# Kernel tuning notes

Hardware: AMD Instinct MI355X
Metric: run time of the kernel (lower is better)

The kernel has to match this reference:

```python
import jax, jax.numpy as jnp
import numpy as np

DIM = 1024
N_HEAD = 16
HEAD_DIM = DIM // N_HEAD
B, T = 2, 2048


def setup_inputs() -> dict:
    key = jax.random.key(0)
    ks = jax.random.split(key, 9)
    s = 1.0 / np.sqrt(DIM)
    return {
        "x": jax.random.normal(ks[0], (B, T, DIM), dtype=jnp.float32),
        "Wq": jax.random.normal(ks[1], (DIM, DIM), dtype=jnp.float32) * s,
        "bq": jax.random.normal(ks[2], (DIM,), dtype=jnp.float32) * s,
        "Wk": jax.random.normal(ks[3], (DIM, DIM), dtype=jnp.float32) * s,
        "bk": jax.random.normal(ks[4], (DIM,), dtype=jnp.float32) * s,
        "Wv": jax.random.normal(ks[5], (DIM, DIM), dtype=jnp.float32) * s,
        "bv": jax.random.normal(ks[6], (DIM,), dtype=jnp.float32) * s,
        "Wo": jax.random.normal(ks[7], (DIM, DIM), dtype=jnp.float32) * s,
        "bo": jax.random.normal(ks[8], (DIM,), dtype=jnp.float32) * s,
    }


def reference(x, Wq, bq, Wk, bk, Wv, bv, Wo, bo):
    b, t, d = x.shape
    # torch nn.Linear: y = x @ W.T + b
    Q = x @ Wq.T + bq  # [b, t, d]
    K = x @ Wk.T + bk
    V = x @ Wv.T + bv
    # split heads -> [b, h, t, hd]
    Q = Q.reshape(b, t, N_HEAD, HEAD_DIM).transpose(0, 2, 1, 3)
    K = K.reshape(b, t, N_HEAD, HEAD_DIM).transpose(0, 2, 1, 3)
    V = V.reshape(b, t, N_HEAD, HEAD_DIM).transpose(0, 2, 1, 3)
    scale = 1.0 / jnp.sqrt(jnp.float32(HEAD_DIM))
    score = jnp.einsum('bhqd,bhkd->bhqk', Q, K) * scale  # [b, h, t, t]
    attn = jax.nn.softmax(score, axis=-1)
    # dropout is identity in eval mode
    out = jnp.einsum('bhqk,bhkd->bhqd', attn, V)  # [b, h, t, hd]
    out = out.transpose(0, 2, 1, 3).reshape(b, t, d)
    return out @ Wo.T + bo
```

## Files before the change

### kernel.cpp

```cpp
#include <hip/hip_runtime.h>


#define DIM 1024
#define NH 16
#define HD 64
#define SEQ 2048
#define NROWS 4096
#define NT 32

typedef unsigned short u16;
typedef unsigned int u32;
typedef __bf16 bf16_t;
typedef bf16_t bf16x8 __attribute__((ext_vector_type(8)));
typedef float f32x4 __attribute__((ext_vector_type(4)));
typedef u16 u16x4 __attribute__((ext_vector_type(4)));
typedef u32 u32x2 __attribute__((ext_vector_type(2)));

typedef const __attribute__((address_space(1))) void* gas_ptr;
typedef __attribute__((address_space(3))) void* las_ptr;

#define S_BARRIER() asm volatile("s_barrier" ::: "memory")
#define S_WAITCNT_VM(N) asm volatile("s_waitcnt vmcnt(" #N ")" ::: "memory")

__device__ __forceinline__ void gl_lds16(const void* g, void* lds_wave_base) {
  __builtin_amdgcn_global_load_lds((gas_ptr)g, (las_ptr)lds_wave_base, 16, 0, 0);
}

__device__ __forceinline__ f32x4 mfma_bf16(bf16x8 a, bf16x8 b, f32x4 c) {
  return __builtin_amdgcn_mfma_f32_16x16x32_bf16(a, b, c, 0, 0, 0);
}

__device__ __forceinline__ u32 cvtpk(float lo, float hi) {
  u32 r;
  asm("v_cvt_pk_bf16_f32 %0, %1, %2" : "=v"(r) : "v"(lo), "v"(hi));
  return r;
}

__device__ __forceinline__ u16 bfu(float f) {
  bf16_t b = (bf16_t)f;
  union { bf16_t b; u16 u; } cv; cv.b = b; return cv.u;
}

__device__ __forceinline__ float fexp2(float x) {
#if __has_builtin(__builtin_amdgcn_exp2f)
  return __builtin_amdgcn_exp2f(x);
#else
  return exp2f(x);
#endif
}

#define QSCALE 0.18033688f

__global__ void cvt_all(const float* __restrict__ x,
                        const float* __restrict__ wq, const float* __restrict__ wk,
                        const float* __restrict__ wv, const float* __restrict__ wo,
                        u16* __restrict__ xb,
                        u16* __restrict__ oq, u16* __restrict__ ok,
                        u16* __restrict__ ov, u16* __restrict__ oo) {
  const int bid = blockIdx.x;
  const float* in;
  u16* out;
  float s = 1.0f;
  int off;
  if (bid < 4096) {
    in = x; out = xb; off = bid;
  } else {
    const int wi = (bid - 4096) >> 10;
    off = (bid - 4096) & 1023;
    in = wi == 0 ? wq : wi == 1 ? wk : wi == 2 ? wv : wo;
    out = wi == 0 ? oq : wi == 1 ? ok : wi == 2 ? ov : oo;
    if (wi == 0) s = QSCALE;
  }
  const int i = off * 256 + threadIdx.x;
  float4 v = ((const float4*)in)[i];
  u16x4 o;
  o.x = bfu(v.x * s); o.y = bfu(v.y * s); o.z = bfu(v.z * s); o.w = bfu(v.w * s);
  ((u16x4*)out)[i] = o;
}

__device__ __forceinline__ int xcd_swz(int L, int nwg) {
  return (L & 7) * (nwg >> 3) + (L >> 3);
}

__global__ __launch_bounds__(256, 3) void gemm_qkv(const u16* __restrict__ A,
                                                   const u16* __restrict__ wq,
                                                   const u16* __restrict__ wk,
                                                   const u16* __restrict__ wv,
                                                   const float* __restrict__ bq,
                                                   const float* __restrict__ bk,
                                                   const float* __restrict__ bv,
                                                   u16* __restrict__ Qb,
                                                   u16* __restrict__ Kb,
                                                   u16* __restrict__ Vtb) {
  __shared__ u16 As[3][128 * 32];
  __shared__ u16 Bs[3][128 * 32];
  const int L = blockIdx.y * gridDim.x + blockIdx.x;
  const int swz = xcd_swz(L, gridDim.x * gridDim.y);
  const int bx = swz % gridDim.x, by = swz / gridDim.x;
  const int which = bx >> 3;
  const int col0 = (bx & 7) * 128;
  const u16* W = which == 0 ? wq : which == 1 ? wk : wv;
  const float* bias = which == 0 ? bq : which == 1 ? bk : bv;
  const float bscale = which == 0 ? QSCALE : 1.0f;

  const int t = threadIdx.x, lane = t & 63, w = t >> 6;
  const int row0 = by * 128;
  const int wr = w >> 1, wc = w & 1;
  const int lr = lane & 15, lk = lane >> 4;

  f32x4 acc[4][4] = {};

  auto stage = [&](int k0, int bu) {
#pragma unroll
    for (int i = 0; i < 2; ++i) {
      const int bc = i * 256 + w * 64;
      const int f = bc + lane;
      gl_lds16(A + (size_t)(row0 + (f >> 2)) * DIM + k0 + (f & 3) * 8, &As[bu][bc * 8]);
      gl_lds16(W + (size_t)(col0 + (f >> 2)) * DIM + k0 + (f & 3) * 8, &Bs[bu][bc * 8]);
    }
  };

  stage(0, 0);
  stage(32, 1);
  int bcur = 0, bst = 2;
  for (int k = 0; k < 32; ++k) {
    S_BARRIER();
    if (k + 2 < 32) { stage((k + 2) * 32, bst); S_WAITCNT_VM(8); }
    else if (k + 1 < 32) { S_WAITCNT_VM(4); }
    else { S_WAITCNT_VM(0); }
    S_BARRIER();

    bf16x8 a[4], b[4];
#pragma unroll
    for (int m = 0; m < 4; ++m)
      a[m] = *(const bf16x8*)&As[bcur][(wr * 64 + m * 16 + lr) * 32 + lk * 8];
#pragma unroll
    for (int n = 0; n < 4; ++n)
      b[n] = *(const bf16x8*)&Bs[bcur][(wc * 64 + n * 16 + lr) * 32 + lk * 8];
    __builtin_amdgcn_s_setprio(1);
#pragma unroll
    for (int m = 0; m < 4; ++m)
#pragma unroll
      for (int n = 0; n < 4; ++n)
        acc[m][n] = mfma_bf16(a[m], b[n], acc[m][n]);
    __builtin_amdgcn_s_setprio(0);

    bcur = bcur == 2 ? 0 : bcur + 1;
    bst = bst == 2 ? 0 : bst + 1;
  }

#pragma unroll
  for (int m = 0; m < 4; ++m) {
    const int rowb = row0 + wr * 64 + m * 16 + lk * 4;
#pragma unroll
    for (int n = 0; n < 4; ++n) {
      const int ocol = col0 + wc * 64 + n * 16 + lr;
      const float bc = bias[ocol] * bscale;
      if (which != 2) {
        u16* dst = which == 0 ? Qb : Kb;
#pragma unroll
        for (int r = 0; r < 4; ++r)
          dst[(size_t)(rowb + r) * DIM + ocol] = bfu(acc[m][n][r] + bc);
      } else {
        u16x4 pk;
#pragma unroll
        for (int r = 0; r < 4; ++r) pk[r] = bfu(acc[m][n][r] + bc);
        const size_t idx = ((((size_t)(rowb >> 11) * NH + (ocol >> 6)) * HD + (ocol & 63)) << 11) + (rowb & 2047);
        *(u16x4*)&Vtb[idx] = pk;
      }
    }
  }
}

__global__ __launch_bounds__(256, 2) void gemm_out(const u16* __restrict__ A,
                                                   const u16* __restrict__ W,
                                                   const float* __restrict__ bias,
                                                   float* __restrict__ C) {
  __shared__ u16 As[3][64 * 32];
  __shared__ u16 Bs[3][128 * 32];
  const int L = blockIdx.x;
  const int swz = xcd_swz(L, 512);
  const int row0 = (swz >> 3) * 64, col0 = (swz & 7) * 128;
  const int t = threadIdx.x, lane = t & 63, w = t >> 6;
  const int wr = w >> 1, wc = w & 1;
  const int lr = lane & 15, lk = lane >> 4;

  f32x4 acc[2][4] = {};

  auto stage = [&](int k0, int bu) {
    const int fa = w * 64 + lane;
    gl_lds16(A + (size_t)(row0 + (fa >> 2)) * DIM + k0 + (fa & 3) * 8, &As[bu][w * 512]);
#pragma unroll
    for (int i = 0; i < 2; ++i) {
      const int bc = i * 256 + w * 64;
      const int fb = bc + lane;
      gl_lds16(W + (size_t)(col0 + (fb >> 2)) * DIM + k0 + (fb & 3) * 8, &Bs[bu][bc * 8]);
    }
  };

  stage(0, 0);
  stage(32, 1);
  int bcur = 0, bst = 2;
  for (int k = 0; k < 32; ++k) {
    S_BARRIER();
    if (k + 2 < 32) { stage((k + 2) * 32, bst); S_WAITCNT_VM(6); }
    else if (k + 1 < 32) { S_WAITCNT_VM(3); }
    else { S_WAITCNT_VM(0); }
    S_BARRIER();

    bf16x8 a[2], b[4];
#pragma unroll
    for (int m = 0; m < 2; ++m)
      a[m] = *(const bf16x8*)&As[bcur][(wr * 32 + m * 16 + lr) * 32 + lk * 8];
#pragma unroll
    for (int n = 0; n < 4; ++n)
      b[n] = *(const bf16x8*)&Bs[bcur][(wc * 64 + n * 16 + lr) * 32 + lk * 8];
    __builtin_amdgcn_s_setprio(1);
#pragma unroll
    for (int m = 0; m < 2; ++m)
#pragma unroll
      for (int n = 0; n < 4; ++n)
        acc[m][n] = mfma_bf16(a[m], b[n], acc[m][n]);
    __builtin_amdgcn_s_setprio(0);

    bcur = bcur == 2 ? 0 : bcur + 1;
    bst = bst == 2 ? 0 : bst + 1;
  }

#pragma unroll
  for (int m = 0; m < 2; ++m) {
    const int rowb = row0 + wr * 32 + m * 16 + lk * 4;
#pragma unroll
    for (int n = 0; n < 4; ++n) {
      const int col = col0 + wc * 64 + n * 16 + lr;
      const float bc = bias[col];
#pragma unroll
      for (int r = 0; r < 4; ++r)
        C[(size_t)(rowb + r) * DIM + col] = acc[m][n][r] + bc;
    }
  }
}

__global__ __launch_bounds__(256, 3) void flash_attn(const u16* __restrict__ Q,
                                                     const u16* __restrict__ K,
                                                     const u16* __restrict__ Vt,
                                                     u16* __restrict__ O) {
  __shared__ u16 Ks[2][64 * 64];
  __shared__ u16 Vs[3][64 * 64];
  __shared__ u16 Ps[4][16][64];

  const int t = threadIdx.x, lane = t & 63, w = t >> 6;
  const int L = blockIdx.x;
  const int bh = ((L >> 8) << 3) | (L & 7);
  const int qt = (L >> 3) & 31;
  const int b = bh >> 4, h = bh & 15;
  const int q0 = qt * 64;
  const int lr = lane & 15, lk = lane >> 4;

  const size_t qrow = (size_t)(b * SEQ + q0 + w * 16 + lr);
  bf16x8 qf[2];
  qf[0] = *(const bf16x8*)&Q[qrow * DIM + h * HD + lk * 8];
  qf[1] = *(const bf16x8*)&Q[qrow * DIM + h * HD + lk * 8 + 32];

  bf16x8 ones;
#pragma unroll
  for (int j = 0; j < 8; ++j) ones[j] = (bf16_t)1.0f;

  f32x4 o[4] = {};
  f32x4 lacc = {};

  auto stage = [&](int kt, int kb, int vb) {
#pragma unroll
    for (int i2 = 0; i2 < 2; ++i2) {
      const int bc = i2 * 256 + w * 64;
      const int f = bc + lane;
      const int row = f >> 3, c = f & 7;
      const int cs = c ^ (row & 7);
      gl_lds16(K + (size_t)(b * SEQ + kt + row) * DIM + h * HD + cs * 8, &Ks[kb][bc * 8]);
      gl_lds16(Vt + (((size_t)bh * HD + row) << 11) + kt + cs * 8, &Vs[vb][bc * 8]);
    }
  };

  auto qk = [&](const u16* ks, f32x4 (&s)[4]) {
    __builtin_amdgcn_s_setprio(1);
#pragma unroll
    for (int n = 0; n < 4; ++n) {
      const int row = n * 16 + lr;
#pragma unroll
      for (int kk = 0; kk < 2; ++kk) {
        bf16x8 kf = *(const bf16x8*)&ks[row * 64 + (((lk + kk * 4) ^ (row & 7)) * 8)];
        s[n] = mfma_bf16(kf, qf[kk], s[n]);
      }
    }
    __builtin_amdgcn_s_setprio(0);
  };

  stage(0, 0, 0);
  stage(64, 1, 1);
  S_WAITCNT_VM(4);
  S_BARRIER();
  f32x4 scur[4] = {};
  qk(Ks[0], scur);

  int vb_pv = 0, vb_st = 2;
  const int rx = (lr & 7) << 3;
#pragma unroll 2
  for (int i = 0; i < NT; ++i) {
    S_BARRIER();
    if (i + 2 < NT) { stage((i + 2) * 64, i & 1, vb_st); }
    f32x4 snext[4] = {};
    if (i + 1 < NT) {
      if (i + 2 < NT) { S_WAITCNT_VM(4); } else { S_WAITCNT_VM(0); }
      S_BARRIER();
      qk(Ks[(i + 1) & 1], snext);
    }

    float p[4][4];
#pragma unroll
    for (int n = 0; n < 4; ++n)
#pragma unroll
      for (int r = 0; r < 4; ++r) p[n][r] = fexp2(scur[n][r]);

#pragma unroll
    for (int n = 0; n < 4; ++n) {
      u32x2 d2;
      d2[0] = cvtpk(p[n][0], p[n][1]);
      d2[1] = cvtpk(p[n][2], p[n][3]);
      *(u32x2*)&Ps[w][lr][(n * 16 + lk * 4) ^ rx] = d2;
    }

    const u16* vs = Vs[vb_pv];
    __builtin_amdgcn_s_setprio(1);
#pragma unroll
    for (int kk = 0; kk < 2; ++kk) {
      bf16x8 pa = *(const bf16x8*)&Ps[w][lr][(kk * 32 + lk * 8) ^ rx];
      lacc = mfma_bf16(pa, ones, lacc);
#pragma unroll
      for (int nd = 0; nd < 4; ++nd) {
        const int vrow = nd * 16 + lr;
        bf16x8 vf = *(const bf16x8*)&vs[vrow * 64 + (((lk + kk * 4) ^ (vrow & 7)) * 8)];
        o[nd] = mfma_bf16(pa, vf, o[nd]);
      }
    }
    __builtin_amdgcn_s_setprio(0);

#pragma unroll
    for (int n = 0; n < 4; ++n) scur[n] = snext[n];
    vb_pv = vb_pv == 2 ? 0 : vb_pv + 1;
    vb_st = vb_st == 2 ? 0 : vb_st + 1;
  }

#pragma unroll
  for (int r = 0; r < 4; ++r) {
    const float inv = 1.f / lacc[r];
    const size_t grow = (size_t)(b * SEQ + q0 + w * 16 + lk * 4 + r);
#pragma unroll
    for (int nd = 0; nd < 4; ++nd)
      O[grow * DIM + h * HD + nd * 16 + lr] = bfu(o[nd][r] * inv);
  }
}

extern "C" void kernel_launch(void* const* d_in, const int* in_sizes, int n_in,
                              void* d_out, int out_size, void* d_ws, size_t ws_size,
                              hipStream_t stream) {
  (void)in_sizes; (void)n_in; (void)out_size; (void)ws_size;
  const float* x  = (const float*)d_in[0];
  const float* Wq = (const float*)d_in[1];
  const float* bq = (const float*)d_in[2];
  const float* Wk = (const float*)d_in[3];
  const float* bk = (const float*)d_in[4];
  const float* Wv = (const float*)d_in[5];
  const float* bv = (const float*)d_in[6];
  const float* Wo = (const float*)d_in[7];
  const float* bo = (const float*)d_in[8];

  char* ws = (char*)d_ws;
  u16* xb  = (u16*)(ws + 0);
  u16* wqb = (u16*)(ws + 8388608);
  u16* wkb = (u16*)(ws + 10485760);
  u16* wvb = (u16*)(ws + 12582912);
  u16* wob = (u16*)(ws + 14680064);
  u16* Qb  = (u16*)(ws + 16777216);
  u16* Kb  = (u16*)(ws + 25165824);
  u16* Vtb = (u16*)(ws + 33554432);
  u16* Ob  = (u16*)(ws + 41943040);

  cvt_all<<<8192, 256, 0, stream>>>(x, Wq, Wk, Wv, Wo, xb, wqb, wkb, wvb, wob);

  gemm_qkv<<<dim3(24, NROWS / 128), 256, 0, stream>>>(xb, wqb, wkb, wvb, bq, bk, bv, Qb, Kb, Vtb);

  flash_attn<<<1024, 256, 0, stream>>>(Qb, Kb, Vtb, Ob);

  gemm_out<<<512, 256, 0, stream>>>(Ob, wob, bo, (float*)d_out);
}
```

Baseline: 128.4 us.

## Simplify flash attention to double-buffered K/V with raised occupancy

Replaces the software-pipelined loop, which computed QK for the next tile while doing softmax/PV on the current one and kept triple-buffered V, with a plain double-buffered loop: prefetch the next K/V tile, wait, then compute QK, exp and PV for the current tile. LDS use drops (Vs from 3 to 2 buffers) and launch bounds rise from 3 to 4 blocks per CU to gain occupancy. In exchange it loses the intra-wave overlap of QK with PV, adds a trailing barrier per iteration, and the higher occupancy bound may limit registers.

```diff
diff --git a/kernel.cpp b/kernel.cpp
--- a/kernel.cpp
+++ b/kernel.cpp
@@ -241,12 +241,12 @@
   }
 }
 
-__global__ __launch_bounds__(256, 3) void flash_attn(const u16* __restrict__ Q,
+__global__ __launch_bounds__(256, 4) void flash_attn(const u16* __restrict__ Q,
                                                      const u16* __restrict__ K,
                                                      const u16* __restrict__ Vt,
                                                      u16* __restrict__ O) {
   __shared__ u16 Ks[2][64 * 64];
-  __shared__ u16 Vs[3][64 * 64];
+  __shared__ u16 Vs[2][64 * 64];
   __shared__ u16 Ps[4][16][64];
 
   const int t = threadIdx.x, lane = t & 63, w = t >> 6;
@@ -269,19 +269,29 @@
   f32x4 o[4] = {};
   f32x4 lacc = {};
 
-  auto stage = [&](int kt, int kb, int vb) {
-#pragma unroll
-    for (int i2 = 0; i2 < 2; ++i2) {
-      const int bc = i2 * 256 + w * 64;
+  auto stage = [&](int kt, int bu) {
+#pragma unroll
+    for (int i = 0; i < 2; ++i) {
+      const int bc = i * 256 + w * 64;
       const int f = bc + lane;
       const int row = f >> 3, c = f & 7;
       const int cs = c ^ (row & 7);
-      gl_lds16(K + (size_t)(b * SEQ + kt + row) * DIM + h * HD + cs * 8, &Ks[kb][bc * 8]);
-      gl_lds16(Vt + (((size_t)bh * HD + row) << 11) + kt + cs * 8, &Vs[vb][bc * 8]);
+      gl_lds16(K + (size_t)(b * SEQ + kt + row) * DIM + h * HD + cs * 8, &Ks[bu][bc * 8]);
+      gl_lds16(Vt + (((size_t)bh * HD + row) << 11) + kt + cs * 8, &Vs[bu][bc * 8]);
     }
   };
 
-  auto qk = [&](const u16* ks, f32x4 (&s)[4]) {
+  stage(0, 0);
+  int buf = 0;
+  for (int kt = 0; kt < SEQ; kt += 64) {
+    if (kt + 64 < SEQ) { stage(kt + 64, buf ^ 1); S_WAITCNT_VM(4); }
+    else               { S_WAITCNT_VM(0); }
+    S_BARRIER();
+
+    const u16* ks = Ks[buf];
+    const u16* vs = Vs[buf];
+
+    f32x4 s[4] = {};
     __builtin_amdgcn_s_setprio(1);
 #pragma unroll
     for (int n = 0; n < 4; ++n) {
@@ -293,34 +303,14 @@
       }
     }
     __builtin_amdgcn_s_setprio(0);
-  };
-
-  stage(0, 0, 0);
-  stage(64, 1, 1);
-  S_WAITCNT_VM(4);
-  S_BARRIER();
-  f32x4 scur[4] = {};
-  qk(Ks[0], scur);
-
-  int vb_pv = 0, vb_st = 2;
-  const int rx = (lr & 7) << 3;
-#pragma unroll 2
-  for (int i = 0; i < NT; ++i) {
-    S_BARRIER();
-    if (i + 2 < NT) { stage((i + 2) * 64, i & 1, vb_st); }
-    f32x4 snext[4] = {};
-    if (i + 1 < NT) {
-      if (i + 2 < NT) { S_WAITCNT_VM(4); } else { S_WAITCNT_VM(0); }
-      S_BARRIER();
-      qk(Ks[(i + 1) & 1], snext);
-    }
 
     float p[4][4];
 #pragma unroll
     for (int n = 0; n < 4; ++n)
 #pragma unroll
-      for (int r = 0; r < 4; ++r) p[n][r] = fexp2(scur[n][r]);
-
+      for (int r = 0; r < 4; ++r) p[n][r] = fexp2(s[n][r]);
+
+    const int rx = (lr & 7) << 3;
 #pragma unroll
     for (int n = 0; n < 4; ++n) {
       u32x2 d2;
@@ -329,7 +319,6 @@
       *(u32x2*)&Ps[w][lr][(n * 16 + lk * 4) ^ rx] = d2;
     }
 
-    const u16* vs = Vs[vb_pv];
     __builtin_amdgcn_s_setprio(1);
 #pragma unroll
     for (int kk = 0; kk < 2; ++kk) {
@@ -344,10 +333,8 @@
     }
     __builtin_amdgcn_s_setprio(0);
 
-#pragma unroll
-    for (int n = 0; n < 4; ++n) scur[n] = snext[n];
-    vb_pv = vb_pv == 2 ? 0 : vb_pv + 1;
-    vb_st = vb_st == 2 ? 0 : vb_st + 1;
+    S_BARRIER();
+    buf ^= 1;
   }
 
 #pragma unroll
```

After: 118.3 us. 1.09x faster.
